# Optimization experiments

Measured on AMD Instinct MI355X. Metric: run time of the kernel, lower is better.

## Reference

```python
import jax, jax.numpy as jnp
import numpy as np

B, S_IMG, S_TXT, D, H, HD = 1, 2048, 512, 3072, 24, 128
A_TOK, A_DIM = 4, 1024
S_TOT = S_IMG + S_TXT
EPS = 1e-6
SCALE = 1.0


def _heads(x):
    # [B, S, D] -> [B, H, S, HD]
    return x.reshape(B, -1, H, HD).transpose(0, 2, 1, 3)


def _rms(x, w):
    return x * jax.lax.rsqrt(jnp.mean(x * x, axis=-1, keepdims=True) + EPS) * w


def _rope(x, cos, sin):
    # diffusers apply_rotary_emb, use_real=True, use_real_unbind_dim=-1
    xr = x.reshape(*x.shape[:-1], HD // 2, 2)
    x1, x2 = xr[..., 0], xr[..., 1]
    x_rot = jnp.stack([-x2, x1], axis=-1).reshape(x.shape)
    return x * cos + x_rot * sin


def _sdpa(q, k, v):
    scores = jnp.einsum('bhqd,bhkd->bhqk', q, k) / np.sqrt(HD).astype(np.float32)
    return jnp.einsum('bhqk,bhkd->bhqd', jax.nn.softmax(scores, axis=-1), v)


def setup_inputs() -> dict:
    key = jax.random.key(0)
    ks = jax.random.split(key, 24)
    s = 0.02
    inp = {
        'hidden_states': jax.random.normal(ks[0], (B, S_IMG, D), jnp.float32),
        'encoder_hidden_states': jax.random.normal(ks[1], (B, S_TXT, D), jnp.float32),
        'adapter_embeds': jax.random.normal(ks[2], (B, A_TOK, A_DIM), jnp.float32),
        'freqs_cos': jnp.cos(jax.random.normal(ks[3], (S_TOT, HD), jnp.float32)),
        'freqs_sin': jnp.sin(jax.random.normal(ks[3], (S_TOT, HD), jnp.float32)),
        'Wq': jax.random.normal(ks[4], (D, D), jnp.float32) * s,
        'bq': jnp.zeros((D,), jnp.float32),
        'Wk': jax.random.normal(ks[5], (D, D), jnp.float32) * s,
        'bk': jnp.zeros((D,), jnp.float32),
        'Wv': jax.random.normal(ks[6], (D, D), jnp.float32) * s,
        'bv': jnp.zeros((D,), jnp.float32),
        'norm_q_w': jnp.ones((HD,), jnp.float32),
        'norm_k_w': jnp.ones((HD,), jnp.float32),
        'Wq_add': jax.random.normal(ks[7], (D, D), jnp.float32) * s,
        'bq_add': jnp.zeros((D,), jnp.float32),
        'Wk_add': jax.random.normal(ks[8], (D, D), jnp.float32) * s,
        'bk_add': jnp.zeros((D,), jnp.float32),
        'Wv_add': jax.random.normal(ks[9], (D, D), jnp.float32) * s,
        'bv_add': jnp.zeros((D,), jnp.float32),
        'norm_added_q_w': jnp.ones((HD,), jnp.float32),
        'norm_added_k_w': jnp.ones((HD,), jnp.float32),
        'Wo': jax.random.normal(ks[10], (D, D), jnp.float32) * s,
        'bo': jnp.zeros((D,), jnp.float32),
        'Wo_add': jax.random.normal(ks[11], (D, D), jnp.float32) * s,
        'bo_add': jnp.zeros((D,), jnp.float32),
        'Wk_adapt': jax.random.normal(ks[12], (A_DIM, D), jnp.float32) * s,
        'Wv_adapt': jax.random.normal(ks[13], (A_DIM, D), jnp.float32) * s,
        'block_scaler': jnp.ones((1,), jnp.float32),
    }
    return inp


def reference(hidden_states, encoder_hidden_states, adapter_embeds, freqs_cos, freqs_sin,
              Wq, bq, Wk, bk, Wv, bv, norm_q_w, norm_k_w,
              Wq_add, bq_add, Wk_add, bk_add, Wv_add, bv_add,
              norm_added_q_w, norm_added_k_w, Wo, bo, Wo_add, bo_add,
              Wk_adapt, Wv_adapt, block_scaler):
    # image-token Q/K/V + per-head RMSNorm
    q = _rms(_heads(hidden_states @ Wq + bq), norm_q_w)
    k = _rms(_heads(hidden_states @ Wk + bk), norm_k_w)
    v = _heads(hidden_states @ Wv + bv)
    # text-token Q/K/V + per-head RMSNorm
    eq = _rms(_heads(encoder_hidden_states @ Wq_add + bq_add), norm_added_q_w)
    ek = _rms(_heads(encoder_hidden_states @ Wk_add + bk_add), norm_added_k_w)
    ev = _heads(encoder_hidden_states @ Wv_add + bv_add)
    # joint sequence: [text, image]
    q = jnp.concatenate([eq, q], axis=2)
    k = jnp.concatenate([ek, k], axis=2)
    v = jnp.concatenate([ev, v], axis=2)
    # RoPE on full joint sequence
    q = _rope(q, freqs_cos, freqs_sin)
    k = _rope(k, freqs_cos, freqs_sin)
    # main joint attention
    hs = _sdpa(q, k, v)                                    # [B,H,S_TOT,HD]
    hs = hs.transpose(0, 2, 1, 3).reshape(B, S_TOT, D)
    # adapter cross-attention (vision-direct branch)
    vd_k = _heads(adapter_embeds @ Wk_adapt)               # [B,H,A_TOK,HD]
    vd_v = _heads(adapter_embeds @ Wv_adapt)
    vd = _sdpa(q, vd_k, vd_v)
    vd = vd.transpose(0, 2, 1, 3).reshape(B, S_TOT, D)
    hs = hs + SCALE * (vd * block_scaler)
    # split back and project
    enc_out = hs[:, :S_TXT] @ Wo_add + bo_add
    img_out = hs[:, S_TXT:] @ Wo + bo
    return img_out, enc_out
```

## Files before the change

kernel.cpp:

```cpp
#include <hip/hip_runtime.h>

typedef unsigned short u16;
typedef short s16x8 __attribute__((ext_vector_type(8)));
typedef float f32x4 __attribute__((ext_vector_type(4)));

#define S_TXTC 512
#define S_TOTC 2560
#define DM 3072
#define NH 24
#define HDM 128

__device__ __forceinline__ float b2f(u16 u){ unsigned int i = ((unsigned int)u)<<16; float f; __builtin_memcpy(&f,&i,4); return f; }
__device__ __forceinline__ u16 f2b(float f){ unsigned int i; __builtin_memcpy(&i,&f,4); unsigned int r = i + 0x7FFFu + ((i>>16)&1u); return (u16)(r>>16); }
__device__ __forceinline__ s16x8 pk8(float4 a, float4 b){
  s16x8 r;
  r[0]=(short)f2b(a.x); r[1]=(short)f2b(a.y); r[2]=(short)f2b(a.z); r[3]=(short)f2b(a.w);
  r[4]=(short)f2b(b.x); r[5]=(short)f2b(b.y); r[6]=(short)f2b(b.z); r[7]=(short)f2b(b.w);
  return r;
}
__device__ __forceinline__ void g2l16(const void* g, void* l){
  __builtin_amdgcn_global_load_lds((const __attribute__((address_space(1))) void*)g,
                                   (__attribute__((address_space(3))) void*)l, 16, 0, 0);
}

__global__ __launch_bounds__(256) void fillv(float* __restrict__ p, int n, float v){
  int i = blockIdx.x*256 + threadIdx.x;
  if (i < n) p[i] = v;
}

__global__ __launch_bounds__(256) void cast2(const float* __restrict__ a, const float* __restrict__ b,
                                             u16* __restrict__ dst, int na8, int n8){
  int i = blockIdx.x*256 + threadIdx.x;
  if (i >= n8) return;
  const float* src = (i < na8)? a + (size_t)i*8 : b + (size_t)(i-na8)*8;
  float4 f0 = *(const float4*)src;
  float4 f1 = *(const float4*)(src+4);
  *(s16x8*)(dst + (size_t)i*8) = pk8(f0,f1);
}

__global__ __launch_bounds__(256) void catbias2(const float* __restrict__ b0, const float* __restrict__ b1,
    const float* __restrict__ b2, const float* __restrict__ c0, const float* __restrict__ c1,
    const float* __restrict__ c2, float* __restrict__ dst){
  int i = blockIdx.x*256 + threadIdx.x;
  if (i >= 18432) return;
  int j = (i < 9216)? i : i - 9216;
  const float* s0 = (i<9216)? b0 : c0; const float* s1 = (i<9216)? b1 : c1; const float* s2 = (i<9216)? b2 : c2;
  dst[i] = (j<3072)? s0[j] : (j<6144? s1[j-3072] : s2[j-6144]);
}

__global__ __launch_bounds__(256) void ktrans3(const float* __restrict__ W0, const float* __restrict__ W1,
    const float* __restrict__ W2, u16* __restrict__ D0, u16* __restrict__ D1, u16* __restrict__ D2){
  const float* W = (blockIdx.z==0)? W0 : ((blockIdx.z==1)? W1 : W2);
  u16* Wt = (blockIdx.z==0)? D0 : ((blockIdx.z==1)? D1 : D2);
  __shared__ __align__(16) u16 t[64*72];
  int nt = blockIdx.x*64, kt_ = blockIdx.y*64;
  int tid = threadIdx.x;
  #pragma unroll
  for (int i=0;i<2;i++){
    int q = tid + 256*i;
    int r = q>>3, c8 = (q&7)*8;
    float4 f0 = *(const float4*)(W + (size_t)(kt_+r)*DM + nt + c8);
    float4 f1 = *(const float4*)(W + (size_t)(kt_+r)*DM + nt + c8 + 4);
    *(s16x8*)&t[r*72 + c8] = pk8(f0,f1);
  }
  __syncthreads();
  #pragma unroll
  for (int i=0;i<2;i++){
    int q = tid + 256*i;
    int n = q>>3, k8 = (q&7)*8;
    s16x8 v;
    #pragma unroll
    for (int j=0;j<8;j++) v[j] = (short)t[(k8+j)*72 + n];
    *(s16x8*)(Wt + (size_t)(nt+n)*DM + kt_ + k8) = v;
  }
}

template<int OUT32>
__device__ __forceinline__ void gcore(u16* la, u16* lb,
    const u16* __restrict__ A, const u16* __restrict__ Bt,
    const float* __restrict__ bias, void* __restrict__ Cv,
    int ldc, int rb, int crb, int cb){
  const int K = DM;
  int tid = threadIdx.x, w = tid>>6, l = tid&63, g = l>>4, c16 = l&15;
  int wr = (w>>1)*64, wc = (w&1)*64;
  f32x4 acc[4][4] = {};
  const u16* aL = A  + (size_t)(rb + w*32 + (l>>2))*K + (l&3)*8;
  const u16* bL = Bt + (size_t)(cb + w*32 + (l>>2))*K + (l&3)*8;
  u16* laB = la + w*1024;
  u16* lbB = lb + w*1024;
  for (int ks=0; ks<K; ks+=32){
    g2l16(aL + ks,                laB);
    g2l16(aL + 16*(size_t)K + ks, laB + 512);
    g2l16(bL + ks,                lbB);
    g2l16(bL + 16*(size_t)K + ks, lbB + 512);
    __syncthreads();
    s16x8 af[4], bf[4];
    #pragma unroll
    for (int m=0;m<4;m++) af[m] = *(const s16x8*)&la[(wr + m*16 + c16)*32 + g*8];
    #pragma unroll
    for (int n=0;n<4;n++) bf[n] = *(const s16x8*)&lb[(wc + n*16 + c16)*32 + g*8];
    #pragma unroll
    for (int m=0;m<4;m++)
      #pragma unroll
      for (int n=0;n<4;n++)
        acc[m][n] = __builtin_amdgcn_mfma_f32_16x16x32_bf16(af[m], bf[n], acc[m][n], 0,0,0);
    __syncthreads();
  }
  #pragma unroll
  for (int n=0;n<4;n++){
    int col = cb + wc + n*16 + c16;
    float bv = bias[col];
    #pragma unroll
    for (int m=0;m<4;m++){
      int r0 = crb + wr + m*16 + g*4;
      #pragma unroll
      for (int r=0;r<4;r++){
        float oo = acc[m][n][r] + bv;
        if (OUT32) ((float*)Cv)[(size_t)(r0+r)*ldc + col] = oo;
        else       ((u16*)Cv)[(size_t)(r0+r)*ldc + col] = f2b(oo);
      }
    }
  }
}

__device__ __forceinline__ void xcd_swz(int& bx, int& by){
  int gx = gridDim.x, nwg = gx*gridDim.y;
  int id = blockIdx.y*gx + blockIdx.x;
  int q = nwg>>3;
  int nid = (id&7)*q + (id>>3);
  bx = nid % gx; by = nid / gx;
}

__global__ __launch_bounds__(256) void qkv_gemm(const u16* __restrict__ A, const u16* __restrict__ Bt,
                                                const float* __restrict__ bias, u16* __restrict__ C){
  __shared__ __align__(16) u16 la[4096];
  __shared__ __align__(16) u16 lb[4096];
  int bx, by; xcd_swz(bx, by);
  gcore<0>(la, lb, A, Bt, bias, C, 3*DM, bx*128, bx*128, by*128);
}

__global__ __launch_bounds__(256) void out_gemm(const u16* __restrict__ hsb,
    const u16* __restrict__ woT, const u16* __restrict__ woaT,
    const float* __restrict__ bo, const float* __restrict__ boa, float* __restrict__ out){
  __shared__ __align__(16) u16 la[4096];
  __shared__ __align__(16) u16 lb[4096];
  int bx, by; xcd_swz(bx, by);
  bool txt = (bx < 4);
  int rb = bx*128;
  const u16* Bt = txt? woaT : woT;
  const float* bias = txt? boa : bo;
  float* dst = txt? out + (size_t)2048*DM : out;
  int crb = txt? rb : rb - 512;
  gcore<1>(la, lb, hsb, Bt, bias, dst, DM, rb, crb, by*128);
}

__global__ __launch_bounds__(256) void epi_fused(
    const u16* __restrict__ qkvI, const u16* __restrict__ qkvT,
    const float* __restrict__ nqw, const float* __restrict__ nkw,
    const float* __restrict__ naq, const float* __restrict__ nak,
    const float* __restrict__ fcos, const float* __restrict__ fsin,
    u16* __restrict__ qh, u16* __restrict__ kh, u16* __restrict__ vt){
  __shared__ __align__(16) u16 t[64*136];
  int blk = blockIdx.x;
  if (blk < 30720){
    int wid = blk*4 + (threadIdx.x>>6);
    int lane = threadIdx.x&63;
    int which = wid / (NH*S_TOTC);
    int rem = wid % (NH*S_TOTC);
    int h = rem / S_TOTC, tok = rem % S_TOTC;
    const u16* src = ((tok<S_TXTC)? qkvT + (size_t)tok*(3*DM) : qkvI + (size_t)(tok-S_TXTC)*(3*DM))
                     + which*DM + h*HDM;
    const float* nw = which? ((tok<S_TXTC)? nak : nkw) : ((tok<S_TXTC)? naq : nqw);
    int d = lane*2;
    unsigned int u = *(const unsigned int*)(src + d);
    float x0 = b2f((u16)(u&0xffffu)), x1 = b2f((u16)(u>>16));
    float ss = x0*x0 + x1*x1;
    #pragma unroll
    for (int m=1;m<64;m<<=1) ss += __shfl_xor(ss, m);
    float rr = rsqrtf(ss*(1.f/128.f) + 1e-6f);
    float y0 = x0*rr*nw[d];
    float y1 = x1*rr*nw[d+1];
    float2 cc = *(const float2*)(fcos + (size_t)tok*HDM + d);
    float2 sn = *(const float2*)(fsin + (size_t)tok*HDM + d);
    float sc = which? 1.0f : 0.08838834764831845f;
    float o0 = (y0*cc.x - y1*sn.x)*sc;
    float o1 = (y1*cc.y + y0*sn.y)*sc;
    u16* dst = (which? kh : qh) + ((size_t)h*S_TOTC + tok)*HDM + d;
    *(unsigned int*)dst = (unsigned int)f2b(o0) | ((unsigned int)f2b(o1)<<16);
  } else {
    int bv = blk - 30720;
    int h = bv % NH, tb = bv / NH;
    int tok0 = tb*64, tid = threadIdx.x;
    #pragma unroll
    for (int i=0;i<4;i++){
      int q = tid + 256*i;
      int tr = q>>4, c8 = (q&15)*8;
      int tok = tok0 + tr;
      const u16* src = ((tok<S_TXTC)? qkvT + (size_t)tok*(3*DM) : qkvI + (size_t)(tok-S_TXTC)*(3*DM))
                       + 2*DM + h*HDM;
      *(s16x8*)&t[tr*136 + c8] = *(const s16x8*)(src + c8);
    }
    __syncthreads();
    #pragma unroll
    for (int i=0;i<4;i++){
      int q = tid + 256*i;
      int d = q>>3, j8 = (q&7)*8;
      s16x8 v;
      #pragma unroll
      for (int j=0;j<8;j++) v[j] = (short)t[(j8+j)*136 + d];
      *(s16x8*)(vt + ((size_t)h*HDM + d)*S_TOTC + tok0 + j8) = v;
    }
  }
}

__global__ __launch_bounds__(256) void adapterk(const float* __restrict__ ad, const float* __restrict__ Wk,
        const float* __restrict__ Wv, u16* __restrict__ vdk, u16* __restrict__ vdv){
  int wid = blockIdx.x*4 + (threadIdx.x>>6);
  int lane = threadIdx.x&63;
  int tensor = wid / (4*DM);
  int rem = wid % (4*DM);
  int tok = rem / DM, col = rem % DM;
  const float* Wp = tensor? Wv : Wk;
  float s = 0.f;
  #pragma unroll
  for (int i=0;i<16;i++){
    int k = lane + 64*i;
    s += ad[tok*1024 + k] * Wp[(size_t)k*DM + col];
  }
  #pragma unroll
  for (int m=1;m<64;m<<=1) s += __shfl_xor(s, m);
  if (lane==0){
    int hh = col>>7, d = col&127;
    (tensor? vdv : vdk)[(hh*4+tok)*HDM + d] = f2b(s);
  }
}

__global__ __launch_bounds__(512,2) void attnk(const u16* __restrict__ qh, const u16* __restrict__ kh,
    const u16* __restrict__ vt, const u16* __restrict__ vdk, const u16* __restrict__ vdv,
    const float* __restrict__ bscale, u16* __restrict__ hs){
  __shared__ __align__(16) u16 kts[64*128];
  __shared__ __align__(16) u16 vts[128*64];
  __shared__ __align__(16) u16 pwb[128*64];
  int h = blockIdx.y, qb = blockIdx.x*128;
  int tid = threadIdx.x, w = tid>>6, l = tid&63, g = l>>4, c16 = l&15;
  int qrow = qb + w*16 + c16;
  int c7 = c16&7;
  s16x8 qf[4];
  #pragma unroll
  for (int kc=0;kc<4;kc++) qf[kc] = *(const s16x8*)(qh + ((size_t)h*S_TOTC + qrow)*HDM + kc*32 + g*8);
  f32x4 acc[8];
  #pragma unroll
  for (int dt=0;dt<8;dt++) acc[dt] = f32x4{0.f,0.f,0.f,0.f};
  float m_[4] = {-3e38f,-3e38f,-3e38f,-3e38f};
  float l_[4] = {0.f,0.f,0.f,0.f};
  const u16* khB = kh + (size_t)h*S_TOTC*HDM;
  const u16* vtB = vt + (size_t)h*HDM*S_TOTC;

  auto LOADT = [&](s16x8* kr, s16x8* vr, int kb){
    #pragma unroll
    for (int i=0;i<2;i++){
      int idx = tid + 512*i;
      kr[i] = *(const s16x8*)(khB + (size_t)(kb + (idx>>4))*HDM + (idx&15)*8);
      vr[i] = *(const s16x8*)(vtB + (size_t)(idx>>3)*S_TOTC + kb + (idx&7)*8);
    }
  };
  auto STORET = [&](s16x8* kr, s16x8* vr){
    #pragma unroll
    for (int i=0;i<2;i++){
      int idx = tid + 512*i;
      int krow = idx>>4, kslot = (idx&15) ^ (krow&7);
      *(s16x8*)&kts[krow*128 + kslot*8] = kr[i];
      int vrow = idx>>3, vslot = (idx&7) ^ (vrow&7);
      *(s16x8*)&vts[vrow*64 + vslot*8] = vr[i];
    }
  };
  auto COMPUTE = [&](){
    f32x4 s[4];
    #pragma unroll
    for (int su=0;su<4;su++) s[su] = f32x4{0.f,0.f,0.f,0.f};
    __builtin_amdgcn_s_setprio(1);
    #pragma unroll
    for (int su=0;su<4;su++)
      #pragma unroll
      for (int kc=0;kc<4;kc++){
        s16x8 kf = *(const s16x8*)&kts[(su*16+c16)*128 + ((kc*4+g) ^ c7)*8];
        s[su] = __builtin_amdgcn_mfma_f32_16x16x32_bf16(qf[kc], kf, s[su], 0,0,0);
      }
    __builtin_amdgcn_s_setprio(0);
    float tm[4];
    #pragma unroll
    for (int r=0;r<4;r++)
      tm[r] = fmaxf(fmaxf(s[0][r],s[1][r]), fmaxf(s[2][r],s[3][r]));
    #pragma unroll
    for (int m=1;m<16;m<<=1)
      #pragma unroll
      for (int r=0;r<4;r++) tm[r] = fmaxf(tm[r], __shfl_xor(tm[r], m));
    bool need = !__all(tm[0]<=m_[0]+8.f && tm[1]<=m_[1]+8.f && tm[2]<=m_[2]+8.f && tm[3]<=m_[3]+8.f);
    if (need){
      float corr[4];
      #pragma unroll
      for (int r=0;r<4;r++){
        float mn = fmaxf(m_[r], tm[r]);
        corr[r] = __expf(m_[r]-mn);
        m_[r] = mn;
        l_[r] *= corr[r];
      }
      #pragma unroll
      for (int dt=0;dt<8;dt++)
        #pragma unroll
        for (int r=0;r<4;r++) acc[dt][r] *= corr[r];
    }
    float rs[4];
    #pragma unroll
    for (int r=0;r<4;r++){
      rs[r] = 0.f;
      #pragma unroll
      for (int su=0;su<4;su++){ s[su][r] = __expf(s[su][r]-m_[r]); rs[r] += s[su][r]; }
    }
    #pragma unroll
    for (int m=1;m<16;m<<=1)
      #pragma unroll
      for (int r=0;r<4;r++) rs[r] += __shfl_xor(rs[r], m);
    #pragma unroll
    for (int r=0;r<4;r++) l_[r] += rs[r];
    #pragma unroll
    for (int su=0;su<4;su++){
      int kslot = su*2 + (c16>>3);
      #pragma unroll
      for (int r=0;r<4;r++){
        int prow = w*16 + g*4 + r;
        pwb[prow*64 + (kslot ^ (prow&7))*8 + c7] = f2b(s[su][r]);
      }
    }
    int prow = w*16 + c16;
    s16x8 pf0 = *(const s16x8*)&pwb[prow*64 + ((0+g) ^ c7)*8];
    s16x8 pf1 = *(const s16x8*)&pwb[prow*64 + ((4+g) ^ c7)*8];
    __builtin_amdgcn_s_setprio(1);
    #pragma unroll
    for (int dt=0;dt<8;dt++){
      int vrow = dt*16 + c16;
      s16x8 vf0 = *(const s16x8*)&vts[vrow*64 + ((0+g) ^ c7)*8];
      acc[dt] = __builtin_amdgcn_mfma_f32_16x16x32_bf16(pf0, vf0, acc[dt], 0,0,0);
      s16x8 vf1 = *(const s16x8*)&vts[vrow*64 + ((4+g) ^ c7)*8];
      acc[dt] = __builtin_amdgcn_mfma_f32_16x16x32_bf16(pf1, vf1, acc[dt], 0,0,0);
    }
    __builtin_amdgcn_s_setprio(0);
  };

  s16x8 ka[2], va[2], kb2[2], vb2[2];
  LOADT(ka, va, 0);
  for (int kb=0; kb<S_TOTC; kb+=128){
    STORET(ka, va);
    __syncthreads();
    LOADT(kb2, vb2, kb+64);
    COMPUTE();
    __syncthreads();
    STORET(kb2, vb2);
    __syncthreads();
    if (kb+128 < S_TOTC) LOADT(ka, va, kb+128);
    COMPUTE();
    __syncthreads();
  }

  if (tid < 64){
    int row = tid>>4, slot = (tid&15) ^ (row&7);
    *(s16x8*)&kts[row*128 + slot*8] = *(const s16x8*)(vdk + (h*4+(tid>>4))*HDM + (tid&15)*8);
  } else if (tid < 192){
    int d = tid - 64;
    int sl0 = (0 ^ (d&7))*8;
    #pragma unroll
    for (int key=0;key<4;key++) vts[d*64 + sl0 + key] = vdv[(h*4+key)*HDM + d];
  }
  __syncthreads();
  f32x4 s2 = {0.f,0.f,0.f,0.f};
  #pragma unroll
  for (int kc=0;kc<4;kc++){
    s16x8 kf = *(const s16x8*)&kts[c16*128 + ((kc*4+g) ^ c7)*8];
    s2 = __builtin_amdgcn_mfma_f32_16x16x32_bf16(qf[kc], kf, s2, 0,0,0);
  }
  bool valid = (c16 < 4);
  float m2[4], l2[4];
  #pragma unroll
  for (int r=0;r<4;r++) m2[r] = valid? s2[r] : -3e38f;
  #pragma unroll
  for (int m=1;m<16;m<<=1)
    #pragma unroll
    for (int r=0;r<4;r++) m2[r] = fmaxf(m2[r], __shfl_xor(m2[r], m));
  #pragma unroll
  for (int r=0;r<4;r++){ float p = valid? __expf(s2[r]-m2[r]) : 0.f; s2[r]=p; l2[r]=p; }
  #pragma unroll
  for (int m=1;m<16;m<<=1)
    #pragma unroll
    for (int r=0;r<4;r++) l2[r] += __shfl_xor(l2[r], m);
  #pragma unroll
  for (int r=0;r<4;r++){
    int prow = w*16 + g*4 + r;
    int s0 = (c16>>3) ^ (prow&7);
    int s1 = (2 + (c16>>3)) ^ (prow&7);
    pwb[prow*64 + s0*8 + c7] = f2b(s2[r]);
    pwb[prow*64 + s1*8 + c7] = (u16)0;
  }
  int prow2 = w*16 + c16;
  s16x8 pf2 = *(const s16x8*)&pwb[prow2*64 + (g ^ c7)*8];
  f32x4 a2[8];
  #pragma unroll
  for (int dt=0;dt<8;dt++) a2[dt] = f32x4{0.f,0.f,0.f,0.f};
  #pragma unroll
  for (int dt=0;dt<8;dt++){
    int vrow = dt*16 + c16;
    s16x8 vf = *(const s16x8*)&vts[vrow*64 + (g ^ c7)*8];
    a2[dt] = __builtin_amdgcn_mfma_f32_16x16x32_bf16(pf2, vf, a2[dt], 0,0,0);
  }
  float sb = bscale[0];
  float rl[4], rl2[4];
  #pragma unroll
  for (int r=0;r<4;r++){ rl[r] = 1.f/l_[r]; rl2[r] = sb/l2[r]; }
  #pragma unroll
  for (int dt=0;dt<8;dt++)
    #pragma unroll
    for (int r=0;r<4;r++){
      int tok = qb + w*16 + g*4 + r;
      int col = h*HDM + dt*16 + c16;
      hs[(size_t)tok*DM + col] = f2b(acc[dt][r]*rl[r] + a2[dt][r]*rl2[r]);
    }
}

extern "C" void kernel_launch(void* const* d_in, const int* in_sizes, int n_in,
                              void* d_out, int out_size, void* d_ws, size_t ws_size,
                              hipStream_t stream){
  static const int expect[28] = {
    6291456, 1572864, 4096, 327680, 327680,
    9437184, 3072, 9437184, 3072, 9437184, 3072, 128, 128,
    9437184, 3072, 9437184, 3072, 9437184, 3072, 128, 128,
    9437184, 3072, 9437184, 3072, 3145728, 3145728, 1 };
  bool ok = (n_in == 28);
  if (ok) for (int i=0;i<28;i++) if (in_sizes[i] != expect[i]) { ok = false; break; }
  if (!ok){ fillv<<<(out_size+255)/256,256,0,stream>>>((float*)d_out, out_size, 7.0f); return; }
  if (ws_size < 119611392ull){ fillv<<<(out_size+255)/256,256,0,stream>>>((float*)d_out, out_size, 9.0f); return; }

  const float* hidden = (const float*)d_in[0];
  const float* enc    = (const float*)d_in[1];
  const float* adapt  = (const float*)d_in[2];
  const float* fcos   = (const float*)d_in[3];
  const float* fsin   = (const float*)d_in[4];
  const float* Wq  = (const float*)d_in[5];  const float* bq  = (const float*)d_in[6];
  const float* Wk  = (const float*)d_in[7];  const float* bk  = (const float*)d_in[8];
  const float* Wv  = (const float*)d_in[9];  const float* bv  = (const float*)d_in[10];
  const float* nqw = (const float*)d_in[11]; const float* nkw = (const float*)d_in[12];
  const float* Wqa = (const float*)d_in[13]; const float* bqa = (const float*)d_in[14];
  const float* Wka = (const float*)d_in[15]; const float* bka = (const float*)d_in[16];
  const float* Wva = (const float*)d_in[17]; const float* bva = (const float*)d_in[18];
  const float* naq = (const float*)d_in[19]; const float* nak = (const float*)d_in[20];
  const float* Wo  = (const float*)d_in[21]; const float* bo  = (const float*)d_in[22];
  const float* Woa = (const float*)d_in[23]; const float* boa = (const float*)d_in[24];
  const float* Wkad = (const float*)d_in[25]; const float* Wvad = (const float*)d_in[26];
  const float* bsc  = (const float*)d_in[27];
  float* out = (float*)d_out;

  char* ws = (char*)d_ws;
  u16* wt3   = (u16*)(ws);
  u16* kh    = (u16*)(ws);
  u16* vth   = (u16*)(ws + 15728640);
  u16* vdk   = (u16*)(ws + 31457280);
  u16* vdv   = (u16*)(ws + 31481856);
  u16* woaT  = (u16*)(ws + 33554432);
  u16* hbf   = (u16*)(ws + 56623104);
  u16* ebf   = (u16*)(ws + 69206016);
  u16* qh    = (u16*)(ws + 56623104);
  u16* qkvI  = (u16*)(ws + 72351744);
  u16* hsb   = (u16*)(ws + 72351744);
  u16* woT   = (u16*)(ws + 88080384);
  u16* qkvT  = (u16*)(ws + 110100480);
  float* biasA = (float*)(ws + 119537664);
  float* biasB = (float*)(ws + 119574528);

  cast2<<<3840,256,0,stream>>>(hidden, enc, hbf, 786432, 983040);
  catbias2<<<72,256,0,stream>>>(bq,bk,bv, bqa,bka,bva, biasA);
  ktrans3<<<dim3(48,48,3),256,0,stream>>>(Wq, Wk, Wv, wt3, wt3 + (size_t)DM*DM, wt3 + (size_t)2*DM*DM);
  qkv_gemm<<<dim3(16,72),256,0,stream>>>(hbf, wt3, biasA, qkvI);
  ktrans3<<<dim3(48,48,3),256,0,stream>>>(Wqa, Wka, Wva, wt3, wt3 + (size_t)DM*DM, wt3 + (size_t)2*DM*DM);
  qkv_gemm<<<dim3(4,72),256,0,stream>>>(ebf, wt3, biasB, qkvT);
  epi_fused<<<31680,256,0,stream>>>(qkvI, qkvT, nqw,nkw,naq,nak, fcos,fsin, qh, kh, vth);
  adapterk<<<6144,256,0,stream>>>(adapt, Wkad, Wvad, vdk, vdv);
  attnk<<<dim3(20,24),512,0,stream>>>(qh, kh, vth, vdk, vdv, bsc, hsb);
  ktrans3<<<dim3(48,48,2),256,0,stream>>>(Wo, Woa, Woa, woT, woaT, woaT);
  out_gemm<<<dim3(20,24),256,0,stream>>>(hsb, woT, woaT, bo, boa, out);
}
```

Baseline: 713.2 us.

## Double-buffer attention K/V tiles in LDS via direct global-to-LDS loads

The attention kernel's K/V staging changes. It used to load into registers and then write to LDS, with several barriers per 128-key step. Now `global_load_lds` DMA copies each 64-key tile straight into one of two LDS buffers, applying the same XOR swizzle on the global source address. The next tile is prefetched into the other buffer while the current one is computed, so each 64-key tile needs only one barrier. This removes register staging and the explicit LDS stores, but raises LDS use per block to about 80KB. At two blocks per CU that approaches the LDS capacity, and correctness depends on the DMA loads being waited on before the barrier.

```diff
diff --git a/kernel.cpp b/kernel.cpp
--- a/kernel.cpp
+++ b/kernel.cpp
@@ -238,8 +238,8 @@
 __global__ __launch_bounds__(512,2) void attnk(const u16* __restrict__ qh, const u16* __restrict__ kh,
     const u16* __restrict__ vt, const u16* __restrict__ vdk, const u16* __restrict__ vdv,
     const float* __restrict__ bscale, u16* __restrict__ hs){
-  __shared__ __align__(16) u16 kts[64*128];
-  __shared__ __align__(16) u16 vts[128*64];
+  __shared__ __align__(16) u16 kts[2][64*128];
+  __shared__ __align__(16) u16 vts[2][128*64];
   __shared__ __align__(16) u16 pwb[128*64];
   int h = blockIdx.y, qb = blockIdx.x*128;
   int tid = threadIdx.x, w = tid>>6, l = tid&63, g = l>>4, c16 = l&15;
@@ -256,25 +256,18 @@
   const u16* khB = kh + (size_t)h*S_TOTC*HDM;
   const u16* vtB = vt + (size_t)h*HDM*S_TOTC;
 
-  auto LOADT = [&](s16x8* kr, s16x8* vr, int kb){
-    #pragma unroll
-    for (int i=0;i<2;i++){
-      int idx = tid + 512*i;
-      kr[i] = *(const s16x8*)(khB + (size_t)(kb + (idx>>4))*HDM + (idx&15)*8);
-      vr[i] = *(const s16x8*)(vtB + (size_t)(idx>>3)*S_TOTC + kb + (idx&7)*8);
+  auto STAGE = [&](int buf, int kb){
+    #pragma unroll
+    for (int c=0;c<2;c++){
+      int krow = w*8 + c*4 + (l>>4);
+      int kchunk = (l&15) ^ (krow&7);
+      g2l16(khB + (size_t)(kb + krow)*HDM + kchunk*8, &kts[buf][w*1024 + c*512]);
+      int vrow = w*16 + c*8 + (l>>3);
+      int vchunk = (l&7) ^ (vrow&7);
+      g2l16(vtB + (size_t)vrow*S_TOTC + kb + vchunk*8, &vts[buf][w*1024 + c*512]);
     }
   };
-  auto STORET = [&](s16x8* kr, s16x8* vr){
-    #pragma unroll
-    for (int i=0;i<2;i++){
-      int idx = tid + 512*i;
-      int krow = idx>>4, kslot = (idx&15) ^ (krow&7);
-      *(s16x8*)&kts[krow*128 + kslot*8] = kr[i];
-      int vrow = idx>>3, vslot = (idx&7) ^ (vrow&7);
-      *(s16x8*)&vts[vrow*64 + vslot*8] = vr[i];
-    }
-  };
-  auto COMPUTE = [&](){
+  auto COMPUTE = [&](int buf){
     f32x4 s[4];
     #pragma unroll
     for (int su=0;su<4;su++) s[su] = f32x4{0.f,0.f,0.f,0.f};
@@ -283,7 +276,7 @@
     for (int su=0;su<4;su++)
       #pragma unroll
       for (int kc=0;kc<4;kc++){
-        s16x8 kf = *(const s16x8*)&kts[(su*16+c16)*128 + ((kc*4+g) ^ c7)*8];
+        s16x8 kf = *(const s16x8*)&kts[buf][(su*16+c16)*128 + ((kc*4+g) ^ c7)*8];
         s[su] = __builtin_amdgcn_mfma_f32_16x16x32_bf16(qf[kc], kf, s[su], 0,0,0);
       }
     __builtin_amdgcn_s_setprio(0);
@@ -339,43 +332,38 @@
     #pragma unroll
     for (int dt=0;dt<8;dt++){
       int vrow = dt*16 + c16;
-      s16x8 vf0 = *(const s16x8*)&vts[vrow*64 + ((0+g) ^ c7)*8];
+      s16x8 vf0 = *(const s16x8*)&vts[buf][vrow*64 + ((0+g) ^ c7)*8];
       acc[dt] = __builtin_amdgcn_mfma_f32_16x16x32_bf16(pf0, vf0, acc[dt], 0,0,0);
-      s16x8 vf1 = *(const s16x8*)&vts[vrow*64 + ((4+g) ^ c7)*8];
+      s16x8 vf1 = *(const s16x8*)&vts[buf][vrow*64 + ((4+g) ^ c7)*8];
       acc[dt] = __builtin_amdgcn_mfma_f32_16x16x32_bf16(pf1, vf1, acc[dt], 0,0,0);
     }
     __builtin_amdgcn_s_setprio(0);
   };
 
-  s16x8 ka[2], va[2], kb2[2], vb2[2];
-  LOADT(ka, va, 0);
-  for (int kb=0; kb<S_TOTC; kb+=128){
-    STORET(ka, va);
+  STAGE(0, 0);
+  __syncthreads();
+  int cur = 0;
+  for (int kb=0; kb<S_TOTC; kb+=64){
+    if (kb+64 < S_TOTC) STAGE(cur^1, kb+64);
+    COMPUTE(cur);
     __syncthreads();
-    LOADT(kb2, vb2, kb+64);
-    COMPUTE();
-    __syncthreads();
-    STORET(kb2, vb2);
-    __syncthreads();
-    if (kb+128 < S_TOTC) LOADT(ka, va, kb+128);
-    COMPUTE();
-    __syncthreads();
+    cur ^= 1;
   }
 
   if (tid < 64){
     int row = tid>>4, slot = (tid&15) ^ (row&7);
-    *(s16x8*)&kts[row*128 + slot*8] = *(const s16x8*)(vdk + (h*4+(tid>>4))*HDM + (tid&15)*8);
+    *(s16x8*)&kts[0][row*128 + slot*8] = *(const s16x8*)(vdk + (h*4+(tid>>4))*HDM + (tid&15)*8);
   } else if (tid < 192){
     int d = tid - 64;
-    int sl0 = (0 ^ (d&7))*8;
-    #pragma unroll
-    for (int key=0;key<4;key++) vts[d*64 + sl0 + key] = vdv[(h*4+key)*HDM + d];
+    int sl0 = (d&7)*8;
+    #pragma unroll
+    for (int key=0;key<4;key++) vts[0][d*64 + sl0 + key] = vdv[(h*4+key)*HDM + d];
   }
   __syncthreads();
   f32x4 s2 = {0.f,0.f,0.f,0.f};
   #pragma unroll
   for (int kc=0;kc<4;kc++){
-    s16x8 kf = *(const s16x8*)&kts[c16*128 + ((kc*4+g) ^ c7)*8];
+    s16x8 kf = *(const s16x8*)&kts[0][c16*128 + ((kc*4+g) ^ c7)*8];
     s2 = __builtin_amdgcn_mfma_f32_16x16x32_bf16(qf[kc], kf, s2, 0,0,0);
   }
   bool valid = (c16 < 4);
@@ -408,7 +396,7 @@
   #pragma unroll
   for (int dt=0;dt<8;dt++){
     int vrow = dt*16 + c16;
-    s16x8 vf = *(const s16x8*)&vts[vrow*64 + (g ^ c7)*8];
+    s16x8 vf = *(const s16x8*)&vts[0][vrow*64 + (g ^ c7)*8];
     a2[dt] = __builtin_amdgcn_mfma_f32_16x16x32_bf16(pf2, vf, a2[dt], 0,0,0);
   }
   float sb = bscale[0];
```

Measured after the change: 681.2 us. -4.5%, faster.
